# Kernel optimization log

Measured on AMD Instinct MI355X. Metric: run time of the kernel, lower is better.

## Reference

```python
import jax, jax.numpy as jnp
import numpy as np

B, S_IN, IN_DIM, HID, H, W = 256, 2, 2304, 512, 7, 7
SCALE = 1.0 / float(np.sqrt(HID))


def setup_inputs() -> dict:
    key = jax.random.key(0)
    ks = jax.random.split(key, 13)
    w = lambda k, shp: (jax.random.normal(k, shp, dtype=jnp.float32) * 0.02)
    return {
        "status": jax.random.normal(ks[0], (B, S_IN), dtype=jnp.float32),
        "rois": jax.random.uniform(ks[1], (B, 5), dtype=jnp.float32),
        "bbox_feat": jax.random.normal(ks[2], (B, IN_DIM, 1, H, W), dtype=jnp.float32),
        "conv_w": w(ks[3], (HID, IN_DIM, 3, 3)),
        "q1_w": w(ks[4], (HID, S_IN + 4)),
        "k1_w": w(ks[5], (HID, HID)),
        "k2_w": w(ks[6], (HID, HID)),
        "v1_w": w(ks[7], (HID, HID)),
        "v2_w": w(ks[8], (HID, HID)),
        "proj1_w": w(ks[9], (HID, HID)),
        "proj1_b": jnp.zeros((HID,), dtype=jnp.float32),
        "proj2_w": w(ks[10], (HID, HID)),
        "proj2_b": jnp.zeros((HID,), dtype=jnp.float32),
    }


def reference(status, rois, bbox_feat, conv_w, q1_w, k1_w, k2_w, v1_w, v2_w,
              proj1_w, proj1_b, proj2_w, proj2_b):
    x = bbox_feat[:, :, 0]  # squeeze(2) -> [B, IN_DIM, H, W]
    feat = jax.lax.conv_general_dilated(
        x, conv_w, window_strides=(1, 1), padding="SAME",
        dimension_numbers=("NCHW", "OIHW", "NCHW"))  # [B, HID, H, W]
    b, c, h, w_ = feat.shape
    hw = h * w_
    feat_seq = feat.reshape(b, c, hw).transpose(0, 2, 1)  # [B, HW, HID]
    st = jnp.concatenate([status, rois[:, 1:]], axis=1)   # [B, status_dim]
    # query is identical at every spatial position (status broadcast over HW),
    # so attention rows are identical -> compute once per batch element.
    q = st @ q1_w.T  # [B, HID] (forward uses q1 for both branches; q2 is dead code)

    def branch(k_w, v_w, p_w, p_b):
        k = feat_seq @ k_w.T                      # [B, HW, HID]
        v = feat_seq @ v_w.T                      # [B, HW, HID]
        logits = jnp.einsum("bd,bnd->bn", q, k) * SCALE
        att = jax.nn.softmax(logits, axis=-1)     # [B, HW]
        virt = jnp.einsum("bn,bnd->bd", att, v)   # [B, HID]
        virt = virt @ p_w.T + p_b                 # proj (dropout = identity in eval)
        out = feat_seq + virt[:, None, :]         # residual, broadcast over HW
        return out.transpose(0, 2, 1).reshape(b, c, h, w_)[:, :, None]  # [B,HID,1,H,W]

    out1 = branch(k1_w, v1_w, proj1_w, proj1_b)
    out2 = branch(k2_w, v2_w, proj2_w, proj2_b)
    return (out1, out2)
```

## Files before the change

kernel.cpp:

```cpp
#include <hip/hip_runtime.h>
#include <hip/hip_bf16.h>
#include <stdint.h>

#define CIN   2304
#define HID_  512
#define NP    12544
#define OUT1  6422528

typedef float  f32x4 __attribute__((ext_vector_type(4)));
typedef short  s16x8 __attribute__((ext_vector_type(8)));

__device__ __forceinline__ uint16_t f2bf(float f) {
  uint32_t x = __builtin_bit_cast(uint32_t, f);
  return (uint16_t)((x + 0x7FFFu + ((x >> 16) & 1u)) >> 16);
}
__device__ __forceinline__ float bf2f(uint16_t u) {
  return __builtin_bit_cast(float, ((uint32_t)u) << 16);
}
__device__ __forceinline__ void gload16(const void* g, void* l) {
  __builtin_amdgcn_global_load_lds((const __attribute__((address_space(1))) void*)g,
                                   (__attribute__((address_space(3))) void*)l, 16, 0, 0);
}

__global__ __launch_bounds__(256) void prep_all_k(const float* __restrict__ xs,
    const float* __restrict__ cw, const float* __restrict__ q1w,
    const float* __restrict__ k1w, const float* __restrict__ k2w,
    const float* __restrict__ v1w, const float* __restrict__ v2w,
    const float* __restrict__ p1w, const float* __restrict__ p2w,
    uint16_t* __restrict__ xT, uint16_t* __restrict__ Wt,
    float* __restrict__ A, float* __restrict__ PVt) {
  __shared__ __align__(16) char sm[18448];
  const int tid = threadIdx.x;
  const int bi = blockIdx.x;
  if (bi < 9216) {
    float* t = (float*)sm;
    const int cg = bi % 36, b = bi / 36;
    const int c0 = cg * 64;
    const float* src = xs + ((size_t)b * CIN + c0) * 49;
    for (int i = tid; i < 3136; i += 256) t[i] = src[i];
    __syncthreads();
    for (int j = tid; j < 392; j += 256) {
      const int s = j >> 3, cq = j & 7;
      union { uint16_t us[8]; uint4 v; } pk;
#pragma unroll
      for (int q = 0; q < 8; ++q) pk.us[q] = f2bf(t[(cq * 8 + q) * 49 + s]);
      *(uint4*)(xT + ((size_t)(b * 49 + s) * CIN + c0 + cq * 8)) = pk.v;
    }
  } else if (bi < 18432) {
    float* t = (float*)sm;
    const int rest = bi - 9216;
    const int cg = rest % 18, o = rest / 18;
    const int c0 = cg * 128;
    const float* src = cw + ((size_t)o * CIN + c0) * 9;
    for (int i = tid; i < 1152; i += 256) t[i] = src[i];
    __syncthreads();
    if (tid < 144) {
      const int tp = tid >> 4, c8 = tid & 15;
      union { uint16_t us[8]; uint4 v; } pk;
#pragma unroll
      for (int q = 0; q < 8; ++q) pk.us[q] = f2bf(t[(c8 * 8 + q) * 9 + tp]);
      *(uint4*)(Wt + ((size_t)(tp * HID_ + o) * CIN + c0 + c8 * 8)) = pk.v;
    }
  } else if (bi < 18448) {
    float* q1s = (float*)sm;
    float (*red)[6][64] = (float(*)[6][64])(sm + 12288);
    const int rest = bi - 18432;
    const int e0 = (rest & 7) * 64, ib = rest >> 3;
    const int g = tid >> 6, l = tid & 63;
    for (int i = tid; i < 3072; i += 256) q1s[i] = q1w[i];
    __syncthreads();
    const float* kw = (ib ? k2w : k1w) + e0 + l;
    float acc[6] = {};
#pragma unroll 4
    for (int d = g * 128; d < (g + 1) * 128; ++d) {
      const float kv = kw[(size_t)d * 512];
#pragma unroll
      for (int j = 0; j < 6; ++j) acc[j] += q1s[d * 6 + j] * kv;
    }
#pragma unroll
    for (int j = 0; j < 6; ++j) red[g][j][l] = acc[j];
    __syncthreads();
    for (int i2 = tid; i2 < 384; i2 += 256) {
      const int j = i2 >> 6, l2 = i2 & 63;
      A[(ib * 6 + j) * 512 + e0 + l2] =
          red[0][j][l2] + red[1][j][l2] + red[2][j][l2] + red[3][j][l2];
    }
  } else {
    float* Av  = (float*)sm;
    float* Bpt = (float*)(sm + 8192);
    const int rest = bi - 18448;
    const int ibz = rest >> 6, r2 = rest & 63;
    const int d0 = (r2 & 7) * 64, e0 = (r2 >> 3) * 64;
    const float* vw = ibz ? v2w : v1w;
    const float* pw = ibz ? p2w : p1w;
    const int tx = tid & 15, ty = tid >> 4;
    float acc[4][4] = {};
    for (int m0 = 0; m0 < 512; m0 += 32) {
      __syncthreads();
      for (int i = tid; i < 2048; i += 256) {
        Av[i] = vw[(size_t)(m0 + (i >> 6)) * 512 + e0 + (i & 63)];
        Bpt[(i & 31) * 68 + (i >> 5)] = pw[(size_t)(d0 + (i >> 5)) * 512 + m0 + (i & 31)];
      }
      __syncthreads();
#pragma unroll 4
      for (int mm = 0; mm < 32; ++mm) {
        const float4 bv = *(const float4*)&Bpt[mm * 68 + tx * 4];
        const float4 av = *(const float4*)&Av[mm * 64 + ty * 4];
        const float a0[4] = {av.x, av.y, av.z, av.w};
        const float b0[4] = {bv.x, bv.y, bv.z, bv.w};
#pragma unroll
        for (int ee = 0; ee < 4; ++ee)
#pragma unroll
          for (int dd = 0; dd < 4; ++dd) acc[ee][dd] += a0[ee] * b0[dd];
      }
    }
#pragma unroll
    for (int ee = 0; ee < 4; ++ee) {
      float4 r; r.x = acc[ee][0]; r.y = acc[ee][1]; r.z = acc[ee][2]; r.w = acc[ee][3];
      *(float4*)&PVt[ibz * 262144 + (size_t)(e0 + ty * 4 + ee) * 512 + d0 + tx * 4] = r;
    }
  }
}

#define LDSX1  11520
#define LDSW   23040
#define LDSZ   47616
__global__ __launch_bounds__(256) void conv_k(const uint16_t* __restrict__ xT,
    const uint16_t* __restrict__ Wt, uint16_t* __restrict__ feat0,
    uint16_t* __restrict__ feat1) {
  __shared__ __align__(16) char lds[47632];
  const int tid = threadIdx.x;
  const int wid = tid >> 6;
  const int lane = tid & 63;
  const int g16 = (lane >> 4) << 4;
  const int l15 = lane & 15;
  const int ww = wid & 1, wm = wid >> 1;

  const int idx = blockIdx.x;
  const int sp = idx & 1;
  const int bn = (idx >> 1) & 3;
  const int bm = idx >> 3;
  const int n0 = bm * 128;
  const int o0 = bn * 128;
  const int c0 = sp * 36;

  const int rb0 = (wm * 64 + l15) * 80 + 640 + g16;
  int maskb[4];
#pragma unroll
  for (int m = 0; m < 4; ++m) {
    const int p = (n0 + wm * 64 + m * 16 + l15) % 49;
    const int y = p / 7, xx = p - y * 7;
    int mb = 0;
#pragma unroll
    for (int t = 0; t < 9; ++t) {
      const int yy = y + t / 3 - 1, xc = xx + t % 3 - 1;
      if (yy >= 0 && yy < 7 && xc >= 0 && xc < 7) mb |= 1 << t;
    }
    maskb[m] = mb;
  }

  const int wb0 = ww * 4096 + l15 * 64 + (g16 ^ (((l15 >> 1) & 3) << 4));

  const char* WtB = (const char*)Wt;
  const char* xTB = (const char*)xT;
  int wsrc[2];
  const int wdstb = wid * 1024;
#pragma unroll
  for (int j = 0; j < 2; ++j) {
    const int slot = j * 256 + tid;
    const int row = slot >> 2, unit = slot & 3;
    const int lu = unit ^ ((row >> 1) & 3);
    wsrc[j] = (o0 + row) * (CIN * 2) + lu * 16;
  }
  int xsrc[3], xv[3];
#pragma unroll
  for (int k = 0; k < 3; ++k) {
    const int slot = k * 256 + tid;
    xv[k] = slot < 720;
    const int row = slot / 5;
    int unit = slot - row * 5; if (unit > 3) unit = 3;
    int nr = n0 - 8 + row;
    nr = nr < 0 ? 0 : (nr > NP - 1 ? NP - 1 : nr);
    xsrc[k] = nr * (CIN * 2) + unit * 16;
  }

  if (tid < 4) *(int*)(lds + LDSZ + tid * 4) = 0;
  __syncthreads();

  {
    const char* xb = xTB + (size_t)c0 * 64;
    if (xv[0]) gload16(xb + xsrc[0], lds + wdstb);
    if (xv[1]) gload16(xb + xsrc[1], lds + 4096 + wdstb);
    if (xv[2]) gload16(xb + xsrc[2], lds + 8192 + wdstb);
    const char* wp0 = WtB + (size_t)c0 * 64;
    gload16(wp0 + wsrc[0], lds + LDSW + wdstb);
    gload16(wp0 + wsrc[1], lds + LDSW + 4096 + wdstb);
    const char* wp1 = WtB + 2359296 + (size_t)c0 * 64;
    gload16(wp1 + wsrc[0], lds + LDSW + 8192 + wdstb);
    gload16(wp1 + wsrc[1], lds + LDSW + 8192 + 4096 + wdstb);
  }

  f32x4 acc[4][4] = {};

#define WISS(TTN, CCO) { \
    const char* wb_ = WtB + (size_t)(TTN) * 2359296 + (size_t)(cc + (CCO)) * 64; \
    const int wo_ = LDSW + ((TTN) % 3) * 8192 + wdstb; \
    gload16(wb_ + wsrc[0], lds + wo_); \
    gload16(wb_ + wsrc[1], lds + wo_ + 4096); }

#define XISS { \
    const char* xb_ = xTB + (size_t)(cc + 1) * 64; \
    const int xo_ = ((cc + 1) & 1) * 11520 + wdstb; \
    if (xv[0]) gload16(xb_ + xsrc[0], lds + xo_); \
    if (xv[1]) gload16(xb_ + xsrc[1], lds + xo_ + 4096); \
    if (xv[2]) gload16(xb_ + xsrc[2], lds + xo_ + 8192); }

#define TAP(TT, VM, ISSUES) \
    asm volatile("s_waitcnt vmcnt(" VM ")" ::: "memory"); \
    __builtin_amdgcn_s_barrier(); \
    __builtin_amdgcn_sched_barrier(0); \
    ISSUES \
    { \
      const int wof_ = LDSW + ((TT) % 3) * 8192; \
      s16x8 bfr_[4]; \
      _Pragma("unroll") \
      for (int n_ = 0; n_ < 4; ++n_) \
        bfr_[n_] = *(const s16x8*)(lds + wof_ + wb0 + n_ * 1024); \
      __builtin_amdgcn_s_setprio(1); \
      _Pragma("unroll") \
      for (int m_ = 0; m_ < 4; ++m_) { \
        const int off_ = m_ * 1280 + (((TT) / 3 - 1) * 7 + ((TT) % 3 - 1)) * 80; \
        const int ab_ = ((maskb[m_] >> (TT)) & 1) ? (rb0 + xsel) : (LDSZ - off_); \
        const s16x8 af_ = *(const s16x8*)(lds + ab_ + off_); \
        _Pragma("unroll") \
        for (int n_ = 0; n_ < 4; ++n_) \
          acc[m_][n_] = __builtin_amdgcn_mfma_f32_16x16x32_bf16(af_, bfr_[n_], acc[m_][n_], 0, 0, 0); \
      } \
      __builtin_amdgcn_s_setprio(0); \
    }

#pragma unroll 1
  for (int cc = c0; cc < c0 + 35; ++cc) {
    const int xsel = (cc & 1) * 11520;
    TAP(0, "2", WISS(2, 0) XISS)
    TAP(1, "5", WISS(3, 0))
    TAP(2, "5", WISS(4, 0))
    TAP(3, "2", WISS(5, 0))
    TAP(4, "2", WISS(6, 0))
    TAP(5, "2", WISS(7, 0))
    TAP(6, "2", WISS(8, 0))
    TAP(7, "2", WISS(0, 1))
    TAP(8, "2", WISS(1, 1))
  }
  {
    const int cc = c0 + 35;
    const int xsel = (cc & 1) * 11520;
    TAP(0, "2", WISS(2, 0))
    TAP(1, "2", WISS(3, 0))
    TAP(2, "2", WISS(4, 0))
    TAP(3, "2", WISS(5, 0))
    TAP(4, "2", WISS(6, 0))
    TAP(5, "2", WISS(7, 0))
    TAP(6, "2", WISS(8, 0))
    TAP(7, "2", )
    TAP(8, "0", )
  }
#undef TAP
#undef WISS
#undef XISS

  uint16_t* fb = (sp ? feat1 : feat0) +
                 ((size_t)(n0 + wm * 64)) * HID_ + o0 + ww * 64;
  const int g4 = (lane >> 4) * 4;
#pragma unroll
  for (int m = 0; m < 4; ++m)
#pragma unroll
    for (int n = 0; n < 4; ++n)
#pragma unroll
      for (int r = 0; r < 4; ++r)
        fb[(m * 16 + g4 + r) * HID_ + n * 16 + l15] = f2bf(acc[m][n][r]);
}

#define FLP 520
__global__ __launch_bounds__(256) void att_k(const uint16_t* __restrict__ feat0,
    const uint16_t* __restrict__ feat1,
    const float* __restrict__ status, const float* __restrict__ rois,
    const float* __restrict__ A, const float* __restrict__ PVt,
    const float* __restrict__ pb1, const float* __restrict__ pb2,
    float* __restrict__ out) {
  __shared__ uint16_t fl[49 * FLP];
  __shared__ float qk[512];
  __shared__ float attv[64];
  __shared__ float fbar[512];
  __shared__ float v2[512];
  __shared__ float part[256];
  const int tid = threadIdx.x;
  const int b = blockIdx.x >> 1, ib = blockIdx.x & 1;

  const uint4* s0 = (const uint4*)(feat0 + (size_t)b * 25088);
  const uint4* s1 = (const uint4*)(feat1 + (size_t)b * 25088);
  for (int i = tid; i < 3136; i += 256) {
    const int n = i >> 6, e8 = (i & 63) << 3;
    union { uint16_t us[8]; uint4 v; } a, c, r;
    a.v = s0[i]; c.v = s1[i];
#pragma unroll
    for (int q = 0; q < 8; ++q) r.us[q] = f2bf(bf2f(a.us[q]) + bf2f(c.us[q]));
    *(uint4*)&fl[n * FLP + e8] = r.v;
  }
  float st6[6];
  st6[0] = status[b * 2]; st6[1] = status[b * 2 + 1];
#pragma unroll
  for (int j = 0; j < 4; ++j) st6[2 + j] = rois[b * 5 + 1 + j];
  for (int e = tid; e < 512; e += 256) {
    const float* Ai = A + ib * 3072;
    float s = 0.f;
#pragma unroll
    for (int j = 0; j < 6; ++j) s += st6[j] * Ai[j * 512 + e];
    qk[e] = s;
  }
  __syncthreads();

  if (tid < 196) {
    const int n = tid >> 2;
    const int e0 = (tid & 3) * 128;
    float s = 0.f;
    for (int e = e0; e < e0 + 128; ++e) s += bf2f(fl[n * FLP + e]) * qk[e];
    part[tid] = s;
  }
  __syncthreads();
  if (tid < 64) {
    float l = -1e30f;
    if (tid < 49)
      l = 0.044194173824159216f *
          (part[tid * 4] + part[tid * 4 + 1] + part[tid * 4 + 2] + part[tid * 4 + 3]);
    float mx = l;
#pragma unroll
    for (int o = 32; o > 0; o >>= 1) mx = fmaxf(mx, __shfl_xor(mx, o, 64));
    const float ex = (tid < 49) ? __expf(l - mx) : 0.f;
    float sm = ex;
#pragma unroll
    for (int o = 32; o > 0; o >>= 1) sm += __shfl_xor(sm, o, 64);
    if (tid < 49) attv[tid] = ex / sm;
  }
  __syncthreads();
  for (int e = tid; e < 512; e += 256) {
    float s = 0.f;
#pragma unroll 7
    for (int n = 0; n < 49; ++n) s += attv[n] * bf2f(fl[n * FLP + e]);
    fbar[e] = s;
  }
  __syncthreads();
  for (int d = tid; d < 512; d += 256) {
    const float* P = PVt + ib * 262144 + d;
    float s = (ib ? pb2 : pb1)[d];
#pragma unroll 8
    for (int e = 0; e < 512; ++e) s += P[(size_t)e * 512] * fbar[e];
    v2[d] = s;
  }
  __syncthreads();
  float* ob = out + (size_t)ib * OUT1 + (size_t)b * 25088;
  for (int w = tid; w < 25088; w += 256) {
    const int c = w / 49, p = w - c * 49;
    ob[w] = bf2f(fl[p * FLP + c]) + v2[c];
  }
}

extern "C" void kernel_launch(void* const* d_in, const int* in_sizes, int n_in,
                              void* d_out, int out_size, void* d_ws, size_t ws_size,
                              hipStream_t stream) {
  const float* status = (const float*)d_in[0];
  const float* rois   = (const float*)d_in[1];
  const float* bbox   = (const float*)d_in[2];
  const float* convw  = (const float*)d_in[3];
  const float* q1w    = (const float*)d_in[4];
  const float* k1w    = (const float*)d_in[5];
  const float* k2w    = (const float*)d_in[6];
  const float* v1w    = (const float*)d_in[7];
  const float* v2w    = (const float*)d_in[8];
  const float* p1w    = (const float*)d_in[9];
  const float* p1b    = (const float*)d_in[10];
  const float* p2w    = (const float*)d_in[11];
  const float* p2b    = (const float*)d_in[12];
  float* out = (float*)d_out;
  char* ws = (char*)d_ws;
  uint16_t* xT    = (uint16_t*)(ws);
  uint16_t* Wt    = (uint16_t*)(ws + 57802752);
  uint16_t* feat0 = (uint16_t*)(ws + 79036416);
  uint16_t* feat1 = (uint16_t*)(ws + 91881472);
  float*    PVt   = (float*)(ws + 104726528);
  float*    A     = (float*)(ws + 106823680);
  if (ws_size < 106848256) return;

  hipLaunchKernelGGL(prep_all_k, dim3(18576), dim3(256), 0, stream,
                     bbox, convw, q1w, k1w, k2w, v1w, v2w, p1w, p2w, xT, Wt, A, PVt);
  hipLaunchKernelGGL(conv_k, dim3(784), dim3(256), 0, stream, xT, Wt, feat0, feat1);
  hipLaunchKernelGGL(att_k,  dim3(512), dim3(256), 0, stream, feat0, feat1,
                     status, rois, A, PVt, p1b, p2b, out);
}
```

Measured before the change: 487.5 us.

## Load conv weights directly into registers in fragment layout, drop weight LDS staging

The weight prep kernel now writes conv weights in a per-tap, per-32-channel-chunk layout that matches the MFMA B-fragment, so the conv kernel can load each wave's weight fragments straight from global memory into registers with double buffering. This removes the LDS weight buffers and the per-tap barriers, leaving one barrier per input-channel chunk for the activation tile. LDS use falls to about 23 KB and launch bounds now request 3 blocks per CU. The input transpose copy is also vectorised to float4. The cost is that weight loads now wait on global or L2 latency in the MFMA loop, with no LDS sharing of weights between waves.

```diff
diff --git a/kernel.cpp b/kernel.cpp
--- a/kernel.cpp
+++ b/kernel.cpp
@@ -36,8 +36,8 @@
     float* t = (float*)sm;
     const int cg = bi % 36, b = bi / 36;
     const int c0 = cg * 64;
-    const float* src = xs + ((size_t)b * CIN + c0) * 49;
-    for (int i = tid; i < 3136; i += 256) t[i] = src[i];
+    const float4* src = (const float4*)(xs + ((size_t)b * CIN + c0) * 49);
+    for (int i = tid; i < 784; i += 256) ((float4*)t)[i] = src[i];
     __syncthreads();
     for (int j = tid; j < 392; j += 256) {
       const int s = j >> 3, cq = j & 7;
@@ -56,10 +56,12 @@
     __syncthreads();
     if (tid < 144) {
       const int tp = tid >> 4, c8 = tid & 15;
+      const int cc = (c0 >> 5) + (c8 >> 2);
+      const int k0 = (c8 & 3) * 8;
       union { uint16_t us[8]; uint4 v; } pk;
 #pragma unroll
       for (int q = 0; q < 8; ++q) pk.us[q] = f2bf(t[(c8 * 8 + q) * 9 + tp]);
-      *(uint4*)(Wt + ((size_t)(tp * HID_ + o) * CIN + c0 + c8 * 8)) = pk.v;
+      *(uint4*)(Wt + (((size_t)(tp * 72 + cc) * 512 + o) * 32 + k0)) = pk.v;
     }
   } else if (bi < 18448) {
     float* q1s = (float*)sm;
@@ -123,12 +125,11 @@
 }
 
 #define LDSX1  11520
-#define LDSW   23040
-#define LDSZ   47616
-__global__ __launch_bounds__(256) void conv_k(const uint16_t* __restrict__ xT,
-    const uint16_t* __restrict__ Wt, uint16_t* __restrict__ feat0,
+#define LDSZ   23040
+__global__ __launch_bounds__(256, 3) void conv_k(const uint16_t* __restrict__ xT,
+    const uint16_t* __restrict__ Wt2, uint16_t* __restrict__ feat0,
     uint16_t* __restrict__ feat1) {
-  __shared__ __align__(16) char lds[47632];
+  __shared__ __align__(16) char lds[23056];
   const int tid = threadIdx.x;
   const int wid = tid >> 6;
   const int lane = tid & 63;
@@ -159,19 +160,8 @@
     maskb[m] = mb;
   }
 
-  const int wb0 = ww * 4096 + l15 * 64 + (g16 ^ (((l15 >> 1) & 3) << 4));
-
-  const char* WtB = (const char*)Wt;
+  const char* wbase = (const char*)Wt2 + ((size_t)(o0 + ww * 64 + l15)) * 64 + g16;
   const char* xTB = (const char*)xT;
-  int wsrc[2];
-  const int wdstb = wid * 1024;
-#pragma unroll
-  for (int j = 0; j < 2; ++j) {
-    const int slot = j * 256 + tid;
-    const int row = slot >> 2, unit = slot & 3;
-    const int lu = unit ^ ((row >> 1) & 3);
-    wsrc[j] = (o0 + row) * (CIN * 2) + lu * 16;
-  }
   int xsrc[3], xv[3];
 #pragma unroll
   for (int k = 0; k < 3; ++k) {
@@ -187,87 +177,76 @@
   if (tid < 4) *(int*)(lds + LDSZ + tid * 4) = 0;
   __syncthreads();
 
-  {
-    const char* xb = xTB + (size_t)c0 * 64;
-    if (xv[0]) gload16(xb + xsrc[0], lds + wdstb);
-    if (xv[1]) gload16(xb + xsrc[1], lds + 4096 + wdstb);
-    if (xv[2]) gload16(xb + xsrc[2], lds + 8192 + wdstb);
-    const char* wp0 = WtB + (size_t)c0 * 64;
-    gload16(wp0 + wsrc[0], lds + LDSW + wdstb);
-    gload16(wp0 + wsrc[1], lds + LDSW + 4096 + wdstb);
-    const char* wp1 = WtB + 2359296 + (size_t)c0 * 64;
-    gload16(wp1 + wsrc[0], lds + LDSW + 8192 + wdstb);
-    gload16(wp1 + wsrc[1], lds + LDSW + 8192 + 4096 + wdstb);
-  }
-
-  f32x4 acc[4][4] = {};
-
-#define WISS(TTN, CCO) { \
-    const char* wb_ = WtB + (size_t)(TTN) * 2359296 + (size_t)(cc + (CCO)) * 64; \
-    const int wo_ = LDSW + ((TTN) % 3) * 8192 + wdstb; \
-    gload16(wb_ + wsrc[0], lds + wo_); \
-    gload16(wb_ + wsrc[1], lds + wo_ + 4096); }
-
-#define XISS { \
-    const char* xb_ = xTB + (size_t)(cc + 1) * 64; \
-    const int xo_ = ((cc + 1) & 1) * 11520 + wdstb; \
-    if (xv[0]) gload16(xb_ + xsrc[0], lds + xo_); \
-    if (xv[1]) gload16(xb_ + xsrc[1], lds + xo_ + 4096); \
-    if (xv[2]) gload16(xb_ + xsrc[2], lds + xo_ + 8192); }
-
-#define TAP(TT, VM, ISSUES) \
-    asm volatile("s_waitcnt vmcnt(" VM ")" ::: "memory"); \
-    __builtin_amdgcn_s_barrier(); \
-    __builtin_amdgcn_sched_barrier(0); \
-    ISSUES \
-    { \
-      const int wof_ = LDSW + ((TT) % 3) * 8192; \
-      s16x8 bfr_[4]; \
-      _Pragma("unroll") \
-      for (int n_ = 0; n_ < 4; ++n_) \
-        bfr_[n_] = *(const s16x8*)(lds + wof_ + wb0 + n_ * 1024); \
-      __builtin_amdgcn_s_setprio(1); \
+#define XSTAGE(CC1) { \
+    const char* xb_ = xTB + (size_t)(CC1) * 64; \
+    char* xd_ = lds + ((CC1) & 1) * LDSX1 + wid * 1024; \
+    if (xv[0]) gload16(xb_ + xsrc[0], xd_); \
+    if (xv[1]) gload16(xb_ + xsrc[1], xd_ + 4096); \
+    if (xv[2]) gload16(xb_ + xsrc[2], xd_ + 8192); }
+
+#define WLOAD(DST, T, CC) { \
+    const char* p_ = wbase + ((size_t)(T) * 72 + (size_t)(CC)) * 32768; \
+    DST[0] = *(const s16x8*)(p_); \
+    DST[1] = *(const s16x8*)(p_ + 1024); \
+    DST[2] = *(const s16x8*)(p_ + 2048); \
+    DST[3] = *(const s16x8*)(p_ + 3072); }
+
+#define TAPB(TT, XSEL, CUR, ISSUE) \
+    { ISSUE \
       _Pragma("unroll") \
       for (int m_ = 0; m_ < 4; ++m_) { \
         const int off_ = m_ * 1280 + (((TT) / 3 - 1) * 7 + ((TT) % 3 - 1)) * 80; \
-        const int ab_ = ((maskb[m_] >> (TT)) & 1) ? (rb0 + xsel) : (LDSZ - off_); \
+        const int ab_ = ((maskb[m_] >> (TT)) & 1) ? (rb0 + (XSEL)) : (LDSZ - off_); \
         const s16x8 af_ = *(const s16x8*)(lds + ab_ + off_); \
+        __builtin_amdgcn_s_setprio(1); \
         _Pragma("unroll") \
         for (int n_ = 0; n_ < 4; ++n_) \
-          acc[m_][n_] = __builtin_amdgcn_mfma_f32_16x16x32_bf16(af_, bfr_[n_], acc[m_][n_], 0, 0, 0); \
-      } \
-      __builtin_amdgcn_s_setprio(0); \
-    }
+          acc[m_][n_] = __builtin_amdgcn_mfma_f32_16x16x32_bf16(af_, CUR[n_], acc[m_][n_], 0, 0, 0); \
+        __builtin_amdgcn_s_setprio(0); \
+      } }
+
+#define CHUNK_SYNC \
+    asm volatile("s_waitcnt vmcnt(4)" ::: "memory"); \
+    __builtin_amdgcn_s_barrier(); \
+    __builtin_amdgcn_sched_barrier(0);
+
+  XSTAGE(c0);
+  f32x4 acc[4][4] = {};
+  s16x8 wA[4], wB[4];
+  WLOAD(wA, 0, c0);
 
 #pragma unroll 1
-  for (int cc = c0; cc < c0 + 35; ++cc) {
-    const int xsel = (cc & 1) * 11520;
-    TAP(0, "2", WISS(2, 0) XISS)
-    TAP(1, "5", WISS(3, 0))
-    TAP(2, "5", WISS(4, 0))
-    TAP(3, "2", WISS(5, 0))
-    TAP(4, "2", WISS(6, 0))
-    TAP(5, "2", WISS(7, 0))
-    TAP(6, "2", WISS(8, 0))
-    TAP(7, "2", WISS(0, 1))
-    TAP(8, "2", WISS(1, 1))
-  }
-  {
-    const int cc = c0 + 35;
-    const int xsel = (cc & 1) * 11520;
-    TAP(0, "2", WISS(2, 0))
-    TAP(1, "2", WISS(3, 0))
-    TAP(2, "2", WISS(4, 0))
-    TAP(3, "2", WISS(5, 0))
-    TAP(4, "2", WISS(6, 0))
-    TAP(5, "2", WISS(7, 0))
-    TAP(6, "2", WISS(8, 0))
-    TAP(7, "2", )
-    TAP(8, "0", )
-  }
-#undef TAP
-#undef WISS
-#undef XISS
+  for (int i = 0; i < 18; ++i) {
+    const int ccA = c0 + 2 * i, ccB = ccA + 1;
+    CHUNK_SYNC
+    XSTAGE(ccA + 1);
+    __builtin_amdgcn_sched_barrier(0);
+    TAPB(0, 0, wA, WLOAD(wB, 1, ccA))
+    TAPB(1, 0, wB, WLOAD(wA, 2, ccA))
+    TAPB(2, 0, wA, WLOAD(wB, 3, ccA))
+    TAPB(3, 0, wB, WLOAD(wA, 4, ccA))
+    TAPB(4, 0, wA, WLOAD(wB, 5, ccA))
+    TAPB(5, 0, wB, WLOAD(wA, 6, ccA))
+    TAPB(6, 0, wA, WLOAD(wB, 7, ccA))
+    TAPB(7, 0, wB, WLOAD(wA, 8, ccA))
+    TAPB(8, 0, wA, WLOAD(wB, 0, ccB))
+    CHUNK_SYNC
+    if (i < 17) { XSTAGE(ccB + 1); }
+    __builtin_amdgcn_sched_barrier(0);
+    TAPB(0, LDSX1, wB, WLOAD(wA, 1, ccB))
+    TAPB(1, LDSX1, wA, WLOAD(wB, 2, ccB))
+    TAPB(2, LDSX1, wB, WLOAD(wA, 3, ccB))
+    TAPB(3, LDSX1, wA, WLOAD(wB, 4, ccB))
+    TAPB(4, LDSX1, wB, WLOAD(wA, 5, ccB))
+    TAPB(5, LDSX1, wA, WLOAD(wB, 6, ccB))
+    TAPB(6, LDSX1, wB, WLOAD(wA, 7, ccB))
+    TAPB(7, LDSX1, wA, WLOAD(wB, 8, ccB))
+    TAPB(8, LDSX1, wB, if (i < 17) WLOAD(wA, 0, ccB + 1))
+  }
+#undef TAPB
+#undef WLOAD
+#undef XSTAGE
+#undef CHUNK_SYNC
 
   uint16_t* fb = (sp ? feat1 : feat0) +
                  ((size_t)(n0 + wm * 64)) * HID_ + o0 + ww * 64;
```

Result: slower. 746.2 us (+53.1%).

## Move weight-product prep blocks into conv kernel and vectorize feature loads

Applied to the files above, without the earlier changes.

The small q1·K and V·P weight-product blocks move out of the prep kernel and run as extra blocks of the conv kernel, so they can overlap with the conv GEMM rather than sit in prep's tail. The input transpose in prep now loads with float4, and the attention logit dot product reads bf16 features eight at a time through uint4 loads. The extra tail blocks launch after the conv blocks, so they may lengthen the conv kernel's tail if they are scheduled late.

```diff
diff --git a/kernel.cpp b/kernel.cpp
--- a/kernel.cpp
+++ b/kernel.cpp
@@ -22,22 +22,18 @@
                                    (__attribute__((address_space(3))) void*)l, 16, 0, 0);
 }
 
-__global__ __launch_bounds__(256) void prep_all_k(const float* __restrict__ xs,
-    const float* __restrict__ cw, const float* __restrict__ q1w,
-    const float* __restrict__ k1w, const float* __restrict__ k2w,
-    const float* __restrict__ v1w, const float* __restrict__ v2w,
-    const float* __restrict__ p1w, const float* __restrict__ p2w,
-    uint16_t* __restrict__ xT, uint16_t* __restrict__ Wt,
-    float* __restrict__ A, float* __restrict__ PVt) {
-  __shared__ __align__(16) char sm[18448];
+__global__ __launch_bounds__(256) void prep1_k(const float* __restrict__ xs,
+    const float* __restrict__ cw,
+    uint16_t* __restrict__ xT, uint16_t* __restrict__ Wt) {
+  __shared__ __align__(16) char sm[12800];
   const int tid = threadIdx.x;
   const int bi = blockIdx.x;
   if (bi < 9216) {
     float* t = (float*)sm;
     const int cg = bi % 36, b = bi / 36;
     const int c0 = cg * 64;
-    const float* src = xs + ((size_t)b * CIN + c0) * 49;
-    for (int i = tid; i < 3136; i += 256) t[i] = src[i];
+    const float4* src = (const float4*)(xs + ((size_t)b * CIN + c0) * 49);
+    for (int i = tid; i < 784; i += 256) ((float4*)t)[i] = src[i];
     __syncthreads();
     for (int j = tid; j < 392; j += 256) {
       const int s = j >> 3, cq = j & 7;
@@ -46,7 +42,7 @@
       for (int q = 0; q < 8; ++q) pk.us[q] = f2bf(t[(cq * 8 + q) * 49 + s]);
       *(uint4*)(xT + ((size_t)(b * 49 + s) * CIN + c0 + cq * 8)) = pk.v;
     }
-  } else if (bi < 18432) {
+  } else {
     float* t = (float*)sm;
     const int rest = bi - 9216;
     const int cg = rest % 18, o = rest / 18;
@@ -61,10 +57,18 @@
       for (int q = 0; q < 8; ++q) pk.us[q] = f2bf(t[(c8 * 8 + q) * 9 + tp]);
       *(uint4*)(Wt + ((size_t)(tp * HID_ + o) * CIN + c0 + c8 * 8)) = pk.v;
     }
-  } else if (bi < 18448) {
+  }
+}
+
+__device__ __forceinline__ void prep_tail(int rest, int tid, char* sm,
+    const float* __restrict__ q1w,
+    const float* __restrict__ k1w, const float* __restrict__ k2w,
+    const float* __restrict__ v1w, const float* __restrict__ v2w,
+    const float* __restrict__ p1w, const float* __restrict__ p2w,
+    float* __restrict__ A, float* __restrict__ PVt) {
+  if (rest < 16) {
     float* q1s = (float*)sm;
     float (*red)[6][64] = (float(*)[6][64])(sm + 12288);
-    const int rest = bi - 18432;
     const int e0 = (rest & 7) * 64, ib = rest >> 3;
     const int g = tid >> 6, l = tid & 63;
     for (int i = tid; i < 3072; i += 256) q1s[i] = q1w[i];
@@ -88,8 +92,8 @@
   } else {
     float* Av  = (float*)sm;
     float* Bpt = (float*)(sm + 8192);
-    const int rest = bi - 18448;
-    const int ibz = rest >> 6, r2 = rest & 63;
+    const int r0 = rest - 16;
+    const int ibz = r0 >> 6, r2 = r0 & 63;
     const int d0 = (r2 & 7) * 64, e0 = (r2 >> 3) * 64;
     const float* vw = ibz ? v2w : v1w;
     const float* pw = ibz ? p2w : p1w;
@@ -127,16 +131,26 @@
 #define LDSZ   47616
 __global__ __launch_bounds__(256) void conv_k(const uint16_t* __restrict__ xT,
     const uint16_t* __restrict__ Wt, uint16_t* __restrict__ feat0,
-    uint16_t* __restrict__ feat1) {
+    uint16_t* __restrict__ feat1,
+    const float* __restrict__ q1w,
+    const float* __restrict__ k1w, const float* __restrict__ k2w,
+    const float* __restrict__ v1w, const float* __restrict__ v2w,
+    const float* __restrict__ p1w, const float* __restrict__ p2w,
+    float* __restrict__ A, float* __restrict__ PVt) {
   __shared__ __align__(16) char lds[47632];
   const int tid = threadIdx.x;
+  const int bidx = blockIdx.x;
+  if (bidx >= 784) {
+    prep_tail(bidx - 784, tid, lds, q1w, k1w, k2w, v1w, v2w, p1w, p2w, A, PVt);
+    return;
+  }
   const int wid = tid >> 6;
   const int lane = tid & 63;
   const int g16 = (lane >> 4) << 4;
   const int l15 = lane & 15;
   const int ww = wid & 1, wm = wid >> 1;
 
-  const int idx = blockIdx.x;
+  const int idx = bidx;
   const int sp = idx & 1;
   const int bn = (idx >> 1) & 3;
   const int bm = idx >> 3;
@@ -324,7 +338,13 @@
     const int n = tid >> 2;
     const int e0 = (tid & 3) * 128;
     float s = 0.f;
-    for (int e = e0; e < e0 + 128; ++e) s += bf2f(fl[n * FLP + e]) * qk[e];
+#pragma unroll 4
+    for (int e8 = 0; e8 < 128; e8 += 8) {
+      union { uint16_t us[8]; uint4 v; } pk;
+      pk.v = *(const uint4*)&fl[n * FLP + e0 + e8];
+#pragma unroll
+      for (int q = 0; q < 8; ++q) s += bf2f(pk.us[q]) * qk[e0 + e8 + q];
+    }
     part[tid] = s;
   }
   __syncthreads();
@@ -391,9 +411,9 @@
   float*    A     = (float*)(ws + 106823680);
   if (ws_size < 106848256) return;
 
-  hipLaunchKernelGGL(prep_all_k, dim3(18576), dim3(256), 0, stream,
-                     bbox, convw, q1w, k1w, k2w, v1w, v2w, p1w, p2w, xT, Wt, A, PVt);
-  hipLaunchKernelGGL(conv_k, dim3(784), dim3(256), 0, stream, xT, Wt, feat0, feat1);
-  hipLaunchKernelGGL(att_k,  dim3(512), dim3(256), 0, stream, feat0, feat1,
+  hipLaunchKernelGGL(prep1_k, dim3(18432), dim3(256), 0, stream, bbox, convw, xT, Wt);
+  hipLaunchKernelGGL(conv_k,  dim3(928),   dim3(256), 0, stream, xT, Wt, feat0, feat1,
+                     q1w, k1w, k2w, v1w, v2w, p1w, p2w, A, PVt);
+  hipLaunchKernelGGL(att_k,   dim3(512),   dim3(256), 0, stream, feat0, feat1,
                      status, rois, A, PVt, p1b, p2b, out);
 }
```

Result: faster. 405.5 us (-16.8%).
